# Kernel optimization log

Measured on AMD Instinct MI355X. Metric: run time of the kernel, lower is better.

Reference implementation:

```python
import jax, jax.numpy as jnp
import numpy as np

N = 32768      # points (multiple of block_size)
D = 32         # h_dim (dim_per_head, also token feature dim)
H = 8          # num_heads
C = 3          # n_hashes
BS = 128       # block_size
R = 3          # coords_dim
K = 8          # num_w_per_dist
NB = N // BS   # buckets
EPS_LN = 1e-5


def _ln(x, w, b):
    mu = x.mean(-1, keepdims=True)
    var = ((x - mu) ** 2).mean(-1, keepdims=True)
    return (x - mu) * jax.lax.rsqrt(var + EPS_LN) * w + b


def setup_inputs() -> dict:
    key = jax.random.key(0)
    ks = jax.random.split(key, 16)
    s = 0.05
    return {
        "x": jax.random.normal(ks[0], (N, D), jnp.float32),
        "coords": jax.random.uniform(ks[1], (N, R), jnp.float32),
        "combined_shifts": jax.random.randint(ks[2], (C, H, N), 0, 2048),
        "norm1_w": jnp.ones((D,), jnp.float32),
        "norm1_b": jnp.zeros((D,), jnp.float32),
        "wq": s * jax.random.normal(ks[3], (D, H * D), jnp.float32),
        "wk": s * jax.random.normal(ks[4], (D, H * D), jnp.float32),
        "wv": s * jax.random.normal(ks[5], (D, H * D), jnp.float32),
        "w_rpe_w": s * jax.random.normal(ks[6], (H * D, R * K), jnp.float32),
        "alpha": jax.random.normal(ks[7], (H, D + R, C), jnp.float32),  # E2LSH (frozen)
        "out_w": s * jax.random.normal(ks[8], (H * D, D), jnp.float32),
        "out_b": jnp.zeros((D,), jnp.float32),
        "norm2_w": jnp.ones((D,), jnp.float32),
        "norm2_b": jnp.zeros((D,), jnp.float32),
        "ff1_w": s * jax.random.normal(ks[9], (D, D), jnp.float32),
        "ff1_b": jnp.zeros((D,), jnp.float32),
        "ff2_w": s * jax.random.normal(ks[10], (D, D), jnp.float32),
        "ff2_b": jnp.zeros((D,), jnp.float32),
    }


def _to_buckets(v, perm):
    # v: [H, N, d], perm: [C, H, N] -> [C, H, NB, BS, d]
    g = jnp.take_along_axis(v[None], perm[..., None], axis=2)
    return g.reshape(C, H, NB, BS, v.shape[-1])


def _from_buckets(s, inv):
    # s: [C, H, NB, BS, d], inv: [C, H, N] -> [C, H, N, d]
    f = s.reshape(C, H, N, s.shape[-1])
    return jnp.take_along_axis(f, inv[..., None], axis=2)


def _hept_forward(x, coords, combined_shifts, norm1_w, norm1_b, wq, wk, wv,
                  w_rpe_w, alpha, out_w, out_b, norm2_w, norm2_b,
                  ff1_w, ff1_b, ff2_w, ff2_b):
    xn = _ln(x, norm1_w, norm1_b)
    q = (xn @ wq).reshape(N, H, D)
    k = (xn @ wk).reshape(N, H, D)
    v = (xn @ wv).reshape(N, H, D)

    # prep_qk: RPE-derived kernel coordinates
    w = w_rpe_w.reshape(H, D, R, K)                       # (h d) (r k) -> h d r k
    qw = jnp.exp(jnp.minimum(w.sum(axis=1), 50.0)).sum(-1)  # [H, R]
    sqrt_w_r = jnp.sqrt(2.0 * qw)[None] * coords[:, None]    # [N, H, R]
    q_hat = jnp.concatenate([q, sqrt_w_r], axis=-1)          # [N, H, D+R]
    k_hat = jnp.concatenate([k, sqrt_w_r], axis=-1)

    q_hat = jnp.transpose(q_hat, (1, 0, 2))  # [H, N, D+R]
    k_hat = jnp.transpose(k_hat, (1, 0, 2))
    val = jnp.transpose(v, (1, 0, 2))        # [H, N, D]

    # LSH hashing (no-grad in original; outputs only feed integer argsort)
    qh = jax.lax.stop_gradient(jnp.einsum('hnd,hdc->chn', q_hat, alpha))
    kh = jax.lax.stop_gradient(jnp.einsum('hnd,hdc->chn', k_hat, alpha))
    hi = jnp.maximum(qh.max(-1, keepdims=True), kh.max(-1, keepdims=True))
    lo = jnp.minimum(qh.min(-1, keepdims=True), kh.min(-1, keepdims=True))
    hash_shift = hi - lo                                    # [C, H, 1]
    shift = combined_shifts.astype(qh.dtype) * hash_shift
    q_pos = jnp.argsort(qh + shift, axis=-1)                # [C, H, N]
    k_pos = jnp.argsort(kh + shift, axis=-1)

    s_query = _to_buckets(q_hat, q_pos)
    s_key = _to_buckets(k_hat, k_pos)
    s_value = _to_buckets(val, k_pos)

    # kernelized exponential attention within buckets
    q_sq = -0.5 * (s_query ** 2).sum(-1, keepdims=True)
    k_sq = -0.5 * (s_key ** 2).sum(-1, keepdims=True)
    dists = jnp.einsum('chbid,chbjd->chbij', s_query, s_key)
    qk = jnp.exp(jnp.minimum(dists + q_sq + jnp.swapaxes(k_sq, -1, -2), 0.0))
    denom = qk.sum(-1, keepdims=True) + 1e-20
    so = jnp.einsum('chbij,chbjd->chbid', qk, s_value)

    q_rev = jnp.argsort(q_pos, axis=-1)  # inverse permutation
    o = _from_buckets(so, q_rev).sum(0)        # [H, N, D]
    logits = _from_buckets(denom, q_rev).sum(0)  # [H, N, 1]
    out = o / logits

    out = jnp.transpose(out, (1, 0, 2)).reshape(N, H * D) @ out_w + out_b
    x = x + out  # dropout is identity in eval
    xn2 = _ln(x, norm2_w, norm2_b)
    ff = jax.nn.silu(xn2 @ ff1_w + ff1_b) @ ff2_w + ff2_b
    return x + ff


def reference(x, coords, combined_shifts, norm1_w, norm1_b, wq, wk, wv,
              w_rpe_w, alpha, out_w, out_b, norm2_w, norm2_b,
              ff1_w, ff1_b, ff2_w, ff2_b):
    return _hept_forward(x, coords, combined_shifts, norm1_w, norm1_b, wq, wk, wv,
                         w_rpe_w, alpha, out_w, out_b, norm2_w, norm2_b,
                         ff1_w, ff1_b, ff2_w, ff2_b)
```

## Files before the change

### kernel.cpp

```cpp
#include <hip/hip_runtime.h>

#define NPTS 32768
#define DIM 32
#define NH 8
#define NC 3
#define BSZ 128
#define NB 256
#define DH 35
#define DP 36
#define NSEG 24

typedef unsigned long long ull;
typedef __attribute__((ext_vector_type(8))) short bf16x8;
typedef __attribute__((ext_vector_type(4))) float f32x4;

__device__ __forceinline__ unsigned fmap(float f){
  unsigned b = __float_as_uint(f);
  return (b & 0x80000000u) ? ~b : (b | 0x80000000u);
}
__device__ __forceinline__ float funmap(unsigned u){
  unsigned b = (u & 0x80000000u) ? (u & 0x7fffffffu) : ~u;
  return __uint_as_float(b);
}
__device__ __forceinline__ unsigned short f2bf(float f){
  unsigned u = __float_as_uint(f);
  u += 0x7fffu + ((u >> 16) & 1u);
  return (unsigned short)(u >> 16);
}
__device__ __forceinline__ float bf2f(unsigned short h){
  return __uint_as_float(((unsigned)h) << 16);
}
__device__ __forceinline__ unsigned cvtpk_bf16(float a, float b){
  unsigned r;
  asm("v_cvt_pk_bf16_f32 %0, %1, %2" : "=v"(r) : "v"(a), "v"(b));
  return r;
}

__device__ __forceinline__ void cswap(ull& a, ull& b, bool up){
  if ((a > b) == up){ ull t = a; a = b; b = t; }
}
__device__ __forceinline__ void bitonic8_initial(ull r[8], unsigned gbase){
  #pragma unroll
  for (int p = 0; p < 4; ++p){
    bool up = (((gbase + 2*p) & 2) == 0);
    cswap(r[2*p], r[2*p+1], up);
  }
  #pragma unroll
  for (int b = 0; b < 2; ++b){
    bool up = (((gbase + 4*b) & 4) == 0);
    cswap(r[4*b+0], r[4*b+2], up);
    cswap(r[4*b+1], r[4*b+3], up);
    cswap(r[4*b+0], r[4*b+1], up);
    cswap(r[4*b+2], r[4*b+3], up);
  }
  bool up = ((gbase & 8) == 0);
  #pragma unroll
  for (int i = 0; i < 4; ++i) cswap(r[i], r[i+4], up);
  #pragma unroll
  for (int b = 0; b < 2; ++b){
    cswap(r[4*b+0], r[4*b+2], up);
    cswap(r[4*b+1], r[4*b+3], up);
  }
  #pragma unroll
  for (int p = 0; p < 4; ++p) cswap(r[2*p], r[2*p+1], up);
}
__device__ __forceinline__ void bitonic8_finish(ull r[8], bool up){
  #pragma unroll
  for (int i = 0; i < 4; ++i) cswap(r[i], r[i+4], up);
  #pragma unroll
  for (int b = 0; b < 2; ++b){
    cswap(r[4*b+0], r[4*b+2], up);
    cswap(r[4*b+1], r[4*b+3], up);
  }
  #pragma unroll
  for (int p = 0; p < 4; ++p) cswap(r[2*p], r[2*p+1], up);
}

__global__ __launch_bounds__(256) void k_prep(const float* __restrict__ w_rpe,
        float* __restrict__ qw_sqrt, unsigned* __restrict__ slots_hi,
        unsigned* __restrict__ slots_lo){
  int tid = threadIdx.x;
  if (tid < NSEG){ slots_hi[tid] = 0u; slots_lo[tid] = 0xFFFFFFFFu; }
  __shared__ float S[24][8];
  if (tid < 192){
    int hr = tid >> 3, kk = tid & 7;
    int h = hr / 3, r = hr % 3;
    float s = 0.f;
    #pragma unroll
    for (int d = 0; d < DIM; ++d) s += w_rpe[(h*DIM + d)*24 + (r*8 + kk)];
    S[hr][kk] = expf(fminf(s, 50.f));
  }
  __syncthreads();
  if (tid < 24){
    float q = 0.f;
    #pragma unroll
    for (int kk = 0; kk < 8; ++kk) q += S[tid][kk];
    qw_sqrt[tid] = sqrtf(2.f * q);
  }
}

__global__ __launch_bounds__(256, 2) void k_qkv(const float* __restrict__ x,
        const float* __restrict__ n1w, const float* __restrict__ n1b,
        const float* __restrict__ coords, const float* __restrict__ wq,
        const float* __restrict__ wk, const float* __restrict__ wv,
        const float* __restrict__ qw_sqrt, const float* __restrict__ alpha,
        short* __restrict__ qpk, short* __restrict__ kpk, short* __restrict__ vbf,
        float* __restrict__ qh_buf, float* __restrict__ kh_buf,
        unsigned* __restrict__ slots_hi, unsigned* __restrict__ slots_lo){
  __shared__ float W[3][DIM][DIM];
  __shared__ float AL[DH][NC];
  __shared__ float LNW[DIM], LNB[DIM];
  __shared__ uint4 STG[3328];
  int h = blockIdx.y;
  int tid = threadIdx.x;
  for (int idx = tid; idx < 3*DIM*DIM; idx += 256){
    int which = idx >> 10, rem = idx & 1023;
    const float* src = which==0 ? wq : (which==1 ? wk : wv);
    W[which][rem>>5][rem&31] = src[(size_t)(rem>>5)*(NH*DIM) + h*DIM + (rem&31)];
  }
  for (int idx = tid; idx < DH*NC; idx += 256) ((float*)AL)[idx] = alpha[h*DH*NC + idx];
  if (tid < DIM) LNW[tid] = n1w[tid];
  else if (tid < 2*DIM) LNB[tid-DIM] = n1b[tid-DIM];
  __syncthreads();

  int base = blockIdx.x * 256;
  int n = base + tid;

  float xa[32];
  {
    const float4* p = (const float4*)(x + (size_t)n*DIM);
    float4 v[8]; float s = 0.f;
    #pragma unroll
    for (int u = 0; u < 8; ++u){ v[u]=p[u]; s += v[u].x+v[u].y+v[u].z+v[u].w; }
    float mu = s*(1.f/32.f), var = 0.f;
    #pragma unroll
    for (int u = 0; u < 8; ++u){
      float a0=v[u].x-mu,a1=v[u].y-mu,a2=v[u].z-mu,a3=v[u].w-mu;
      var += a0*a0+a1*a1+a2*a2+a3*a3;
    }
    var *= (1.f/32.f);
    float rs = rsqrtf(var + 1e-5f);
    #pragma unroll
    for (int u = 0; u < 8; ++u){
      xa[u*4+0]=(v[u].x-mu)*rs*LNW[u*4+0]+LNB[u*4+0];
      xa[u*4+1]=(v[u].y-mu)*rs*LNW[u*4+1]+LNB[u*4+1];
      xa[u*4+2]=(v[u].z-mu)*rs*LNW[u*4+2]+LNB[u*4+2];
      xa[u*4+3]=(v[u].w-mu)*rs*LNW[u*4+3]+LNB[u*4+3];
    }
  }

  float c0 = qw_sqrt[h*3+0]*coords[(size_t)n*3+0];
  float c1 = qw_sqrt[h*3+1]*coords[(size_t)n*3+1];
  float c2 = qw_sqrt[h*3+2]*coords[(size_t)n*3+2];
  float csq = c0*c0 + c1*c1 + c2*c2;

  uint2* rowp = (uint2*)&STG[tid*13];

  auto do_proj = [&](int which, float (&hp)[3], float& sq, bool dohash){
    #pragma unroll
    for (int j0 = 0; j0 < 32; j0 += 4){
      float4 a = {0,0,0,0};
      #pragma unroll
      for (int d = 0; d < 32; ++d){
        float4 w4 = *(const float4*)&W[which][d][j0];
        a.x += xa[d]*w4.x; a.y += xa[d]*w4.y; a.z += xa[d]*w4.z; a.w += xa[d]*w4.w;
      }
      if (dohash){
        sq += a.x*a.x; sq += a.y*a.y; sq += a.z*a.z; sq += a.w*a.w;
        #pragma unroll
        for (int c = 0; c < 3; ++c){
          float t = hp[c];
          t += a.x*AL[j0][c];   t += a.y*AL[j0+1][c];
          t += a.z*AL[j0+2][c]; t += a.w*AL[j0+3][c];
          hp[c] = t;
        }
      }
      unsigned short hx=f2bf(a.x),hy=f2bf(a.y),hz=f2bf(a.z),hw=f2bf(a.w);
      uint2 hv, lv;
      hv.x = (unsigned)hx | ((unsigned)hy<<16);
      hv.y = (unsigned)hz | ((unsigned)hw<<16);
      lv.x = (unsigned)f2bf(a.x-bf2f(hx)) | ((unsigned)f2bf(a.y-bf2f(hy))<<16);
      lv.y = (unsigned)f2bf(a.z-bf2f(hz)) | ((unsigned)f2bf(a.w-bf2f(hw))<<16);
      rowp[j0/4] = hv;
      rowp[12 + j0/4] = lv;
    }
  };
  auto stage_tail = [&](float x5, float x6){
    unsigned short h0=f2bf(c0),h1=f2bf(c1),h2=f2bf(c2),h5=f2bf(x5),h6=f2bf(x6);
    uint2 z2; z2.x=0; z2.y=0;
    uint2 hv0, hv1, lv0, lv1;
    hv0.x = (unsigned)h0 | ((unsigned)h1<<16);
    hv0.y = (unsigned)h2 | ((unsigned)h5<<16);
    hv1.x = (unsigned)h6; hv1.y = 0;
    lv0.x = (unsigned)f2bf(c0-bf2f(h0)) | ((unsigned)f2bf(c1-bf2f(h1))<<16);
    lv0.y = (unsigned)f2bf(c2-bf2f(h2)) | ((unsigned)f2bf(x5-bf2f(h5))<<16);
    lv1.x = (unsigned)f2bf(x6-bf2f(h6)); lv1.y = 0;
    rowp[8] = hv0; rowp[9] = hv1; rowp[10] = z2; rowp[11] = z2;
    rowp[20] = lv0; rowp[21] = lv1; rowp[22] = z2; rowp[23] = z2;
  };
  auto copy_qk = [&](short* gdst){
    uint4* du = (uint4*)gdst;
    #pragma unroll
    for (int it = 0; it < 12; ++it){
      unsigned g = (unsigned)it*256u + (unsigned)tid;
      unsigned row = g / 12u, k = g % 12u;
      du[g] = STG[row*13u + k];
    }
  };

  float qh[3]={0,0,0}, kh[3]={0,0,0};
  float sq = 0.f, dum = 0.f;

  do_proj(0, qh, sq, true);
  float qsq = -0.5f*(sq + csq);
  stage_tail(1.0f, qsq);
  __syncthreads();
  copy_qk(qpk + ((size_t)h*NPTS + base)*96);
  __syncthreads();

  sq = 0.f;
  do_proj(1, kh, sq, true);
  float ksq = -0.5f*(sq + csq);
  stage_tail(ksq, 1.0f);
  __syncthreads();
  copy_qk(kpk + ((size_t)h*NPTS + base)*96);
  __syncthreads();

  {
    float dh[3];
    uint2* rv = (uint2*)&STG[tid*5];
    #pragma unroll
    for (int j0 = 0; j0 < 32; j0 += 4){
      float4 a = {0,0,0,0};
      #pragma unroll
      for (int d = 0; d < 32; ++d){
        float4 w4 = *(const float4*)&W[2][d][j0];
        a.x += xa[d]*w4.x; a.y += xa[d]*w4.y; a.z += xa[d]*w4.z; a.w += xa[d]*w4.w;
      }
      uint2 hv;
      hv.x = (unsigned)f2bf(a.x) | ((unsigned)f2bf(a.y)<<16);
      hv.y = (unsigned)f2bf(a.z) | ((unsigned)f2bf(a.w)<<16);
      rv[j0/4] = hv;
    }
    (void)dh;
  }
  __syncthreads();
  {
    uint4* dv = (uint4*)(vbf + ((size_t)h*NPTS + base)*32);
    #pragma unroll
    for (int it = 0; it < 4; ++it){
      unsigned g = (unsigned)it*256u + (unsigned)tid;
      unsigned row = g >> 2, k = g & 3u;
      dv[g] = STG[row*5u + k];
    }
  }

  float mx[3], mn[3];
  #pragma unroll
  for (int c = 0; c < 3; ++c){
    float qa_ = qh[c];
    qa_ += c0*AL[32][c]; qa_ += c1*AL[33][c]; qa_ += c2*AL[34][c];
    float ka_ = kh[c];
    ka_ += c0*AL[32][c]; ka_ += c1*AL[33][c]; ka_ += c2*AL[34][c];
    qh_buf[(size_t)(c*NH + h)*NPTS + n] = qa_;
    kh_buf[(size_t)(c*NH + h)*NPTS + n] = ka_;
    mx[c] = fmaxf(qa_, ka_);
    mn[c] = fminf(qa_, ka_);
  }
  #pragma unroll
  for (int c = 0; c < 3; ++c){
    float mx_ = mx[c], mn_ = mn[c];
    #pragma unroll
    for (int off = 1; off <= 32; off <<= 1){
      mx_ = fmaxf(mx_, __shfl_xor(mx_, off));
      mn_ = fminf(mn_, __shfl_xor(mn_, off));
    }
    if ((tid & 63) == 0){
      atomicMax(&slots_hi[c*NH + h], fmap(mx_));
      atomicMin(&slots_lo[c*NH + h], fmap(mn_));
    }
  }
  (void)dum;
}

__global__ __launch_bounds__(1024) void k_sort_pack_local(
        const float* __restrict__ qh_buf, const float* __restrict__ kh_buf,
        const int* __restrict__ shifts,
        const unsigned* __restrict__ slots_hi, const unsigned* __restrict__ slots_lo,
        ull* __restrict__ packed){
  __shared__ ull ld[9216];
  int chunk = blockIdx.x;
  int lst = chunk >> 2;
  int seg = lst < NSEG ? lst : lst - NSEG;
  const float* buf = lst < NSEG ? qh_buf : kh_buf;
  unsigned coff = (unsigned)(chunk & 3) * 8192u;
  float hs = funmap(slots_hi[seg]) - funmap(slots_lo[seg]);
  unsigned tid = threadIdx.x;

  {
    ull r[8];
    unsigned gb = coff + 8u*tid;
    #pragma unroll
    for (int e = 0; e < 8; ++e){
      unsigned n = gb + e;
      size_t gi = (size_t)seg*NPTS + n;
      float key = buf[gi] + (float)shifts[gi] * hs;
      r[e] = ((ull)fmap(key) << 32) | n;
    }
    bitonic8_initial(r, gb);
    #pragma unroll
    for (int e = 0; e < 8; ++e) ld[9u*tid + e] = r[e];
  }
  __syncthreads();

  for (unsigned k = 16; k <= 8192u; k <<= 1){
    for (unsigned j = k >> 1; j >= 8; j >>= 1){
      #pragma unroll
      for (int it = 0; it < 4; ++it){
        unsigned p = tid + 1024u*it;
        unsigned i  = ((p & ~(j-1)) << 1) | (p & (j-1));
        unsigned x2 = i | j;
        bool up = (((coff + i) & k) == 0);
        unsigned pi = i + (i>>3), px = x2 + (x2>>3);
        ull a = ld[pi], b2 = ld[px];
        if ((a > b2) == up){ ld[pi] = b2; ld[px] = a; }
      }
      __syncthreads();
    }
    {
      ull r[8];
      #pragma unroll
      for (int e = 0; e < 8; ++e) r[e] = ld[9u*tid + e];
      bool up = (((coff + 8u*tid) & k) == 0);
      bitonic8_finish(r, up);
      #pragma unroll
      for (int e = 0; e < 8; ++e) ld[9u*tid + e] = r[e];
    }
    __syncthreads();
  }
  size_t base = (size_t)lst*NPTS + coff;
  for (unsigned idx = tid; idx < 8192; idx += 1024)
    packed[base + idx] = ld[idx + (idx>>3)];
}

__global__ __launch_bounds__(1024) void k_sort_local(ull* __restrict__ data,
        unsigned k_lo, unsigned k_hi){
  __shared__ ull ld[9216];
  int chunk = blockIdx.x;
  size_t base = (size_t)chunk * 8192;
  unsigned coff = (unsigned)(chunk & 3) * 8192u;
  unsigned tid = threadIdx.x;
  for (unsigned idx = tid; idx < 8192; idx += 1024)
    ld[idx + (idx>>3)] = data[base + idx];
  __syncthreads();
  for (unsigned k = k_lo; k <= k_hi; k <<= 1){
    unsigned j0 = (k >> 1) < 4096u ? (k >> 1) : 4096u;
    for (unsigned j = j0; j >= 8; j >>= 1){
      #pragma unroll
      for (int it = 0; it < 4; ++it){
        unsigned p = tid + 1024u*it;
        unsigned i  = ((p & ~(j-1)) << 1) | (p & (j-1));
        unsigned x2 = i | j;
        bool up = (((coff + i) & k) == 0);
        unsigned pi = i + (i>>3), px = x2 + (x2>>3);
        ull a = ld[pi], b2 = ld[px];
        if ((a > b2) == up){ ld[pi] = b2; ld[px] = a; }
      }
      __syncthreads();
    }
    {
      ull r[8];
      #pragma unroll
      for (int e = 0; e < 8; ++e) r[e] = ld[9u*tid + e];
      bool up = (((coff + 8u*tid) & k) == 0);
      bitonic8_finish(r, up);
      #pragma unroll
      for (int e = 0; e < 8; ++e) ld[9u*tid + e] = r[e];
    }
    __syncthreads();
  }
  for (unsigned idx = tid; idx < 8192; idx += 1024)
    data[base + idx] = ld[idx + (idx>>3)];
}

__global__ __launch_bounds__(256) void k_sort_global(ull* __restrict__ data,
        unsigned k, unsigned j){
  unsigned t = blockIdx.x*256 + threadIdx.x;
  unsigned seg = t >> 14;
  unsigned p = t & 16383u;
  unsigned i  = ((p & ~(j-1)) << 1) | (p & (j-1));
  unsigned x2 = i | j;
  size_t base = (size_t)seg << 15;
  bool up = ((i & k) == 0);
  ull a = data[base + i], b = data[base + x2];
  if ((a > b) == up){ data[base + i] = b; data[base + x2] = a; }
}

__global__ __launch_bounds__(256) void k_sort_global2(ull* __restrict__ data){
  unsigned t = blockIdx.x*256 + threadIdx.x;
  unsigned seg = t >> 13;
  unsigned i = t & 8191u;
  size_t base = ((size_t)seg << 15) + i;
  ull e0 = data[base], e1 = data[base + 8192], e2 = data[base + 16384], e3 = data[base + 24576];
  cswap(e0, e2, true); cswap(e1, e3, true);
  cswap(e0, e1, true); cswap(e2, e3, true);
  data[base] = e0; data[base + 8192] = e1;
  data[base + 16384] = e2; data[base + 24576] = e3;
}

__global__ __launch_bounds__(512, 8) void k_attn(const short* __restrict__ qpk,
        const short* __restrict__ kpk, const short* __restrict__ vbf,
        const ull* __restrict__ packed, float* __restrict__ o_acc,
        float* __restrict__ logit_acc){
  __shared__ short KP[16384];
  __shared__ short Vt[4096];

  int t = threadIdx.x;
  int blk = blockIdx.x;
  int seg = blk >> 8;
  int b = blk & 255;
  int h = seg & 7;
  const ull* pq = packed + ((size_t)seg << 15) + (size_t)b*BSZ;
  const ull* pk = packed + ((size_t)(NSEG + seg) << 15) + (size_t)b*BSZ;

  int lane = t & 63;
  int w = t >> 6;
  int l15 = lane & 15, g = lane >> 4;
  int qrow = 16*w + l15;

  unsigned iqr = (unsigned)(pq[qrow] & 0xffffffffull);
  const short* qrp = qpk + ((size_t)h*NPTS + iqr)*96;
  bf16x8 qh0 = *(const bf16x8*)&qrp[8*g];
  bf16x8 ql0 = *(const bf16x8*)&qrp[48 + 8*g];
  bf16x8 qh1 = (bf16x8){0,0,0,0,0,0,0,0};
  bf16x8 ql1 = (bf16x8){0,0,0,0,0,0,0,0};
  if (g < 2){
    qh1 = *(const bf16x8*)&qrp[32 + 8*g];
    ql1 = *(const bf16x8*)&qrp[80 + 8*g];
  }

  {
    int r = t >> 2;
    int qd = t & 3;
    unsigned ik = (unsigned)(pk[r] & 0xffffffffull);
    int rowbase = r*64;
    int sw = (r & 7) << 3;
    const short* krp = kpk + ((size_t)h*NPTS + ik)*96;
    if (qd < 3){
      bf16x8 h0 = *(const bf16x8*)&krp[16*qd];
      bf16x8 h1 = *(const bf16x8*)&krp[16*qd + 8];
      bf16x8 l0 = *(const bf16x8*)&krp[48 + 16*qd];
      bf16x8 l1 = *(const bf16x8*)&krp[56 + 16*qd];
      *(bf16x8*)&KP[rowbase + ((16*qd) ^ sw)] = h0;
      *(bf16x8*)&KP[rowbase + ((16*qd + 8) ^ sw)] = h1;
      *(bf16x8*)&KP[8192 + rowbase + ((16*qd) ^ sw)] = l0;
      *(bf16x8*)&KP[8192 + rowbase + ((16*qd + 8) ^ sw)] = l1;
    } else {
      bf16x8 z = (bf16x8){0,0,0,0,0,0,0,0};
      *(bf16x8*)&KP[rowbase + (48 ^ sw)] = z;
      *(bf16x8*)&KP[rowbase + (56 ^ sw)] = z;
      *(bf16x8*)&KP[8192 + rowbase + (48 ^ sw)] = z;
      *(bf16x8*)&KP[8192 + rowbase + (56 ^ sw)] = z;
    }
    const short* vrp = vbf + ((size_t)h*NPTS + ik)*32 + 8*qd;
    bf16x8 vv = *(const bf16x8*)vrp;
    #pragma unroll
    for (int d2 = 0; d2 < 8; ++d2){
      int vd = 8*qd + d2;
      Vt[vd*128 + (r ^ ((vd & 7) << 3))] = vv[d2];
    }
  }
  __syncthreads();

  f32x4 acc[8];
  #pragma unroll
  for (int kt = 0; kt < 8; ++kt) acc[kt] = (f32x4){0.f,0.f,0.f,0.f};
  #pragma unroll
  for (int kt = 0; kt < 8; ++kt){
    int krow = 16*kt + l15;
    int base = krow*64;
    int sw = (krow & 7) << 3;
    bf16x8 ah0 = *(const bf16x8*)&KP[base + ((8*g) ^ sw)];
    bf16x8 ah1 = *(const bf16x8*)&KP[base + ((32 + 8*g) ^ sw)];
    bf16x8 al0 = *(const bf16x8*)&KP[8192 + base + ((8*g) ^ sw)];
    bf16x8 al1 = *(const bf16x8*)&KP[8192 + base + ((32 + 8*g) ^ sw)];
    f32x4 c = acc[kt];
    c = __builtin_amdgcn_mfma_f32_16x16x32_bf16(ah0, qh0, c, 0, 0, 0);
    c = __builtin_amdgcn_mfma_f32_16x16x32_bf16(ah1, qh1, c, 0, 0, 0);
    c = __builtin_amdgcn_mfma_f32_16x16x32_bf16(al0, qh0, c, 0, 0, 0);
    c = __builtin_amdgcn_mfma_f32_16x16x32_bf16(al1, qh1, c, 0, 0, 0);
    c = __builtin_amdgcn_mfma_f32_16x16x32_bf16(ah0, ql0, c, 0, 0, 0);
    c = __builtin_amdgcn_mfma_f32_16x16x32_bf16(ah1, ql1, c, 0, 0, 0);
    acc[kt] = c;
  }

  __syncthreads();

  int qsw = (qrow & 7) << 3;
  float dena = 0.f;
  #pragma unroll
  for (int kt = 0; kt < 8; ++kt){
    f32x4 c = acc[kt];
    float p0 = __expf(fminf(c[0], 0.f));
    float p1 = __expf(fminf(c[1], 0.f));
    float p2 = __expf(fminf(c[2], 0.f));
    float p3 = __expf(fminf(c[3], 0.f));
    dena += p0 + p1 + p2 + p3;
    int key = 16*kt + 4*g;
    uint2 pv;
    pv.x = cvtpk_bf16(p0, p1);
    pv.y = cvtpk_bf16(p2, p3);
    *(uint2*)&KP[qrow*128 + (key ^ qsw)] = pv;
  }

  f32x4 oacc[2];
  oacc[0] = (f32x4){0.f,0.f,0.f,0.f};
  oacc[1] = (f32x4){0.f,0.f,0.f,0.f};
  #pragma unroll
  for (int ks = 0; ks < 4; ++ks){
    bf16x8 pA = *(const bf16x8*)&KP[qrow*128 + ((32*ks + 8*g) ^ qsw)];
    #pragma unroll
    for (int nt = 0; nt < 2; ++nt){
      int vd = 16*nt + l15;
      bf16x8 vB = *(const bf16x8*)&Vt[vd*128 + ((32*ks + 8*g) ^ ((vd&7)<<3))];
      oacc[nt] = __builtin_amdgcn_mfma_f32_16x16x32_bf16(pA, vB, oacc[nt], 0, 0, 0);
    }
  }

  {
    float d = dena;
    d += __shfl_xor(d, 16);
    d += __shfl_xor(d, 32);
    if (lane < 16) atomicAdd(&logit_acc[(size_t)h*NPTS + iqr], d + 1e-20f);
  }
  #pragma unroll
  for (int nt = 0; nt < 2; ++nt){
    f32x4 c = oacc[nt];
    #pragma unroll
    for (int r = 0; r < 4; ++r){
      unsigned iq = (unsigned)__shfl((int)iqr, 4*g + r);
      atomicAdd(&o_acc[((size_t)h*NPTS + iq)*DIM + 16*nt + l15], c[r]);
    }
  }
}

__global__ __launch_bounds__(256) void k_final(const float* __restrict__ x,
        const float* __restrict__ o_acc, const float* __restrict__ logit_acc,
        const float* __restrict__ out_w, const float* __restrict__ out_b,
        const float* __restrict__ n2w, const float* __restrict__ n2b,
        const float* __restrict__ f1w, const float* __restrict__ f1b,
        const float* __restrict__ f2w, const float* __restrict__ f2b,
        float* __restrict__ out){
  __shared__ float OW[256][32];
  __shared__ float F1[32][32];
  __shared__ float F2[32][32];
  int tid = threadIdx.x;
  for (int idx = tid; idx < 256*32; idx += 256) OW[idx/32][idx%32] = out_w[idx];
  for (int idx = tid; idx < 1024; idx += 256){
    F1[idx/32][idx%32] = f1w[idx];
    F2[idx/32][idx%32] = f2w[idx];
  }
  __syncthreads();
  int n = blockIdx.x*256 + tid;
  float attn[32];
  #pragma unroll
  for (int j = 0; j < 32; ++j) attn[j] = out_b[j];
  for (int h = 0; h < 8; ++h){
    float inv = 1.f / logit_acc[(size_t)h*NPTS + n];
    const float4* orow = (const float4*)(o_acc + ((size_t)h*NPTS + n)*DIM);
    #pragma unroll
    for (int u = 0; u < 8; ++u){
      float4 ov = orow[u];
      float vals[4] = {ov.x*inv, ov.y*inv, ov.z*inv, ov.w*inv};
      #pragma unroll
      for (int s = 0; s < 4; ++s){
        const float* wrow = &OW[h*32 + u*4 + s][0];
        #pragma unroll
        for (int j = 0; j < 32; ++j) attn[j] += vals[s] * wrow[j];
      }
    }
  }
  const float* xp = x + (size_t)n*DIM;
  float xr[32]; float s = 0.f;
  #pragma unroll
  for (int d = 0; d < 32; ++d){ xr[d] = xp[d] + attn[d]; s += xr[d]; }
  float mu = s * (1.f/32.f);
  float var = 0.f;
  #pragma unroll
  for (int d = 0; d < 32; ++d){ float dx = xr[d]-mu; var += dx*dx; }
  var *= (1.f/32.f);
  float rs = rsqrtf(var + 1e-5f);
  float xn2[32];
  #pragma unroll
  for (int d = 0; d < 32; ++d) xn2[d] = (xr[d]-mu)*rs*n2w[d] + n2b[d];
  float z[32];
  #pragma unroll
  for (int j = 0; j < 32; ++j) z[j] = f1b[j];
  #pragma unroll
  for (int d = 0; d < 32; ++d){
    float xd = xn2[d];
    const float* wrow = &F1[d][0];
    #pragma unroll
    for (int j = 0; j < 32; ++j) z[j] += xd * wrow[j];
  }
  #pragma unroll
  for (int j = 0; j < 32; ++j) z[j] = z[j] / (1.f + __expf(-z[j]));
  float y[32];
  #pragma unroll
  for (int d = 0; d < 32; ++d) y[d] = f2b[d];
  #pragma unroll
  for (int j = 0; j < 32; ++j){
    float zj = z[j];
    const float* wrow = &F2[j][0];
    #pragma unroll
    for (int d = 0; d < 32; ++d) y[d] += zj * wrow[d];
  }
  float* op = out + (size_t)n*DIM;
  #pragma unroll
  for (int d = 0; d < 32; ++d) op[d] = xr[d] + y[d];
}

extern "C" void kernel_launch(void* const* d_in, const int* in_sizes, int n_in,
                              void* d_out, int out_size, void* d_ws, size_t ws_size,
                              hipStream_t stream){
  const float* x      = (const float*)d_in[0];
  const float* coords = (const float*)d_in[1];
  const int*   shifts = (const int*)d_in[2];
  const float* n1w    = (const float*)d_in[3];
  const float* n1b    = (const float*)d_in[4];
  const float* wq     = (const float*)d_in[5];
  const float* wk     = (const float*)d_in[6];
  const float* wv     = (const float*)d_in[7];
  const float* w_rpe  = (const float*)d_in[8];
  const float* alpha  = (const float*)d_in[9];
  const float* out_w  = (const float*)d_in[10];
  const float* out_b  = (const float*)d_in[11];
  const float* n2w    = (const float*)d_in[12];
  const float* n2b    = (const float*)d_in[13];
  const float* f1w    = (const float*)d_in[14];
  const float* f1b    = (const float*)d_in[15];
  const float* f2w    = (const float*)d_in[16];
  const float* f2b    = (const float*)d_in[17];
  float* out = (float*)d_out;

  char* ws = (char*)d_ws;
  size_t off = 0;
  auto alloc = [&](size_t bytes){ size_t o = off; off += (bytes + 255) & ~(size_t)255; return o; };
  float*    qw_sqrt   = (float*)   (ws + alloc(24*4));
  unsigned* slots_hi  = (unsigned*)(ws + alloc(24*4));
  unsigned* slots_lo  = (unsigned*)(ws + alloc(24*4));
  short*    qpk       = (short*)   (ws + alloc((size_t)NH*NPTS*96*2));
  short*    kpk       = (short*)   (ws + alloc((size_t)NH*NPTS*96*2));
  short*    vbf       = (short*)   (ws + alloc((size_t)NH*NPTS*32*2));
  float*    qh_buf    = (float*)   (ws + alloc((size_t)NSEG*NPTS*4));
  float*    kh_buf    = (float*)   (ws + alloc((size_t)NSEG*NPTS*4));
  ull*      packed    = (ull*)     (ws + alloc((size_t)2*NSEG*NPTS*8));
  float*    o_acc     = (float*)   (ws + alloc((size_t)NH*NPTS*DIM*4));
  float*    logit_acc = (float*)   (ws + alloc((size_t)NH*NPTS*4));
  if (off > ws_size) return;

  hipMemsetAsync(o_acc, 0, (size_t)NH*NPTS*DIM*4, stream);
  hipMemsetAsync(logit_acc, 0, (size_t)NH*NPTS*4, stream);

  k_prep<<<1, 256, 0, stream>>>(w_rpe, qw_sqrt, slots_hi, slots_lo);
  k_qkv<<<dim3(NPTS/256, NH), 256, 0, stream>>>(x, n1w, n1b, coords, wq, wk, wv,
                                                qw_sqrt, alpha, qpk, kpk, vbf,
                                                qh_buf, kh_buf, slots_hi, slots_lo);
  k_sort_pack_local<<<2*NSEG*4, 1024, 0, stream>>>(qh_buf, kh_buf, shifts,
                                                   slots_hi, slots_lo, packed);
  k_sort_global<<<(2*NSEG*16384)/256, 256, 0, stream>>>(packed, 16384u, 8192u);
  k_sort_local<<<2*NSEG*4, 1024, 0, stream>>>(packed, 16384u, 16384u);
  k_sort_global2<<<(2*NSEG*8192)/256, 256, 0, stream>>>(packed);
  k_sort_local<<<2*NSEG*4, 1024, 0, stream>>>(packed, 32768u, 32768u);

  k_attn<<<NSEG*NB, 512, 0, stream>>>(qpk, kpk, vbf, packed, o_acc, logit_acc);
  k_final<<<NPTS/256, 256, 0, stream>>>(x, o_acc, logit_acc, out_w, out_b,
                                        n2w, n2b, f1w, f1b, f2w, f2b, out);
}
```

Baseline: 442.7 us.

## Replace atomic scatter of attention outputs with sorted-order stores and gather

The attention kernel now writes per-bucket outputs and denominators in sorted order (outputs in bf16) instead of atomically adding into per-point accumulators. A new kernel builds the inverse permutation, and the final kernel gathers the three hash contributions per head via that index. This removes the memsets and the float atomics, at the cost of an extra gather pass and bf16 rounding of the partial outputs. Separately, the QKV kernel splits each point across two threads (half the output columns each), using less shared memory and a higher occupancy hint.

```diff
diff --git a/kernel.cpp b/kernel.cpp
--- a/kernel.cpp
+++ b/kernel.cpp
@@ -99,7 +99,7 @@
   }
 }
 
-__global__ __launch_bounds__(256, 2) void k_qkv(const float* __restrict__ x,
+__global__ __launch_bounds__(256, 4) void k_qkv(const float* __restrict__ x,
         const float* __restrict__ n1w, const float* __restrict__ n1b,
         const float* __restrict__ coords, const float* __restrict__ wq,
         const float* __restrict__ wk, const float* __restrict__ wv,
@@ -110,7 +110,7 @@
   __shared__ float W[3][DIM][DIM];
   __shared__ float AL[DH][NC];
   __shared__ float LNW[DIM], LNB[DIM];
-  __shared__ uint4 STG[3328];
+  __shared__ uint4 STG[1664];
   int h = blockIdx.y;
   int tid = threadIdx.x;
   for (int idx = tid; idx < 3*DIM*DIM; idx += 256){
@@ -123,15 +123,17 @@
   else if (tid < 2*DIM) LNB[tid-DIM] = n1b[tid-DIM];
   __syncthreads();
 
-  int base = blockIdx.x * 256;
-  int n = base + tid;
+  int base = blockIdx.x * 128;
+  int tl = tid >> 1;
+  int p  = tid & 1;
+  int n  = base + tl;
 
   float xa[32];
   {
-    const float4* p = (const float4*)(x + (size_t)n*DIM);
+    const float4* pp = (const float4*)(x + (size_t)n*DIM);
     float4 v[8]; float s = 0.f;
     #pragma unroll
-    for (int u = 0; u < 8; ++u){ v[u]=p[u]; s += v[u].x+v[u].y+v[u].z+v[u].w; }
+    for (int u = 0; u < 8; ++u){ v[u]=pp[u]; s += v[u].x+v[u].y+v[u].z+v[u].w; }
     float mu = s*(1.f/32.f), var = 0.f;
     #pragma unroll
     for (int u = 0; u < 8; ++u){
@@ -154,11 +156,12 @@
   float c2 = qw_sqrt[h*3+2]*coords[(size_t)n*3+2];
   float csq = c0*c0 + c1*c1 + c2*c2;
 
-  uint2* rowp = (uint2*)&STG[tid*13];
+  uint2* rowp = (uint2*)&STG[tl*13];
 
   auto do_proj = [&](int which, float (&hp)[3], float& sq, bool dohash){
     #pragma unroll
-    for (int j0 = 0; j0 < 32; j0 += 4){
+    for (int j0l = 0; j0l < 16; j0l += 4){
+      int j0 = p*16 + j0l;
       float4 a = {0,0,0,0};
       #pragma unroll
       for (int d = 0; d < 32; ++d){
@@ -181,8 +184,8 @@
       hv.y = (unsigned)hz | ((unsigned)hw<<16);
       lv.x = (unsigned)f2bf(a.x-bf2f(hx)) | ((unsigned)f2bf(a.y-bf2f(hy))<<16);
       lv.y = (unsigned)f2bf(a.z-bf2f(hz)) | ((unsigned)f2bf(a.w-bf2f(hw))<<16);
-      rowp[j0/4] = hv;
-      rowp[12 + j0/4] = lv;
+      rowp[j0>>2] = hv;
+      rowp[12 + (j0>>2)] = lv;
     }
   };
   auto stage_tail = [&](float x5, float x6){
@@ -201,7 +204,7 @@
   auto copy_qk = [&](short* gdst){
     uint4* du = (uint4*)gdst;
     #pragma unroll
-    for (int it = 0; it < 12; ++it){
+    for (int it = 0; it < 6; ++it){
       unsigned g = (unsigned)it*256u + (unsigned)tid;
       unsigned row = g / 12u, k = g % 12u;
       du[g] = STG[row*13u + k];
@@ -209,28 +212,34 @@
   };
 
   float qh[3]={0,0,0}, kh[3]={0,0,0};
-  float sq = 0.f, dum = 0.f;
+  float sq = 0.f;
 
   do_proj(0, qh, sq, true);
-  float qsq = -0.5f*(sq + csq);
-  stage_tail(1.0f, qsq);
+  {
+    float sqt = sq + __shfl_xor(sq, 1);
+    float qsq = -0.5f*(sqt + csq);
+    if (p == 0) stage_tail(1.0f, qsq);
+  }
   __syncthreads();
   copy_qk(qpk + ((size_t)h*NPTS + base)*96);
   __syncthreads();
 
   sq = 0.f;
   do_proj(1, kh, sq, true);
-  float ksq = -0.5f*(sq + csq);
-  stage_tail(ksq, 1.0f);
+  {
+    float sqt = sq + __shfl_xor(sq, 1);
+    float ksq = -0.5f*(sqt + csq);
+    if (p == 0) stage_tail(ksq, 1.0f);
+  }
   __syncthreads();
   copy_qk(kpk + ((size_t)h*NPTS + base)*96);
   __syncthreads();
 
   {
-    float dh[3];
-    uint2* rv = (uint2*)&STG[tid*5];
-    #pragma unroll
-    for (int j0 = 0; j0 < 32; j0 += 4){
+    uint2* rv = (uint2*)&STG[tl*5];
+    #pragma unroll
+    for (int j0l = 0; j0l < 16; j0l += 4){
+      int j0 = p*16 + j0l;
       float4 a = {0,0,0,0};
       #pragma unroll
       for (int d = 0; d < 32; ++d){
@@ -240,15 +249,14 @@
       uint2 hv;
       hv.x = (unsigned)f2bf(a.x) | ((unsigned)f2bf(a.y)<<16);
       hv.y = (unsigned)f2bf(a.z) | ((unsigned)f2bf(a.w)<<16);
-      rv[j0/4] = hv;
-    }
-    (void)dh;
+      rv[j0>>2] = hv;
+    }
   }
   __syncthreads();
   {
     uint4* dv = (uint4*)(vbf + ((size_t)h*NPTS + base)*32);
     #pragma unroll
-    for (int it = 0; it < 4; ++it){
+    for (int it = 0; it < 2; ++it){
       unsigned g = (unsigned)it*256u + (unsigned)tid;
       unsigned row = g >> 2, k = g & 3u;
       dv[g] = STG[row*5u + k];
@@ -258,14 +266,16 @@
   float mx[3], mn[3];
   #pragma unroll
   for (int c = 0; c < 3; ++c){
-    float qa_ = qh[c];
-    qa_ += c0*AL[32][c]; qa_ += c1*AL[33][c]; qa_ += c2*AL[34][c];
-    float ka_ = kh[c];
-    ka_ += c0*AL[32][c]; ka_ += c1*AL[33][c]; ka_ += c2*AL[34][c];
-    qh_buf[(size_t)(c*NH + h)*NPTS + n] = qa_;
-    kh_buf[(size_t)(c*NH + h)*NPTS + n] = ka_;
-    mx[c] = fmaxf(qa_, ka_);
-    mn[c] = fminf(qa_, ka_);
+    float qt = qh[c] + __shfl_xor(qh[c], 1);
+    qt += c0*AL[32][c]; qt += c1*AL[33][c]; qt += c2*AL[34][c];
+    float kt = kh[c] + __shfl_xor(kh[c], 1);
+    kt += c0*AL[32][c]; kt += c1*AL[33][c]; kt += c2*AL[34][c];
+    if (p == 0){
+      qh_buf[(size_t)(c*NH + h)*NPTS + n] = qt;
+      kh_buf[(size_t)(c*NH + h)*NPTS + n] = kt;
+    }
+    mx[c] = fmaxf(qt, kt);
+    mn[c] = fminf(qt, kt);
   }
   #pragma unroll
   for (int c = 0; c < 3; ++c){
@@ -280,7 +290,6 @@
       atomicMin(&slots_lo[c*NH + h], fmap(mn_));
     }
   }
-  (void)dum;
 }
 
 __global__ __launch_bounds__(1024) void k_sort_pack_local(
@@ -408,10 +417,19 @@
   data[base + 16384] = e2; data[base + 24576] = e3;
 }
 
+__global__ __launch_bounds__(256) void k_qrev(const ull* __restrict__ packed,
+        unsigned* __restrict__ qrev){
+  unsigned t = blockIdx.x*256 + threadIdx.x;
+  unsigned seg = t >> 15;
+  unsigned pos = t & 32767u;
+  unsigned idx = (unsigned)(packed[(size_t)seg*NPTS + pos] & 0xffffffffull);
+  qrev[(size_t)seg*NPTS + idx] = pos;
+}
+
 __global__ __launch_bounds__(512, 8) void k_attn(const short* __restrict__ qpk,
         const short* __restrict__ kpk, const short* __restrict__ vbf,
-        const ull* __restrict__ packed, float* __restrict__ o_acc,
-        float* __restrict__ logit_acc){
+        const ull* __restrict__ packed, unsigned short* __restrict__ o_sorted,
+        float* __restrict__ den_sorted){
   __shared__ short KP[16384];
   __shared__ short Vt[4096];
 
@@ -531,21 +549,23 @@
     float d = dena;
     d += __shfl_xor(d, 16);
     d += __shfl_xor(d, 32);
-    if (lane < 16) atomicAdd(&logit_acc[(size_t)h*NPTS + iqr], d + 1e-20f);
-  }
+    if (lane < 16) den_sorted[(size_t)seg*NPTS + (size_t)b*BSZ + 16*w + l15] = d;
+  }
+  size_t obase = ((size_t)seg*NPTS + (size_t)b*BSZ)*32;
   #pragma unroll
   for (int nt = 0; nt < 2; ++nt){
     f32x4 c = oacc[nt];
     #pragma unroll
     for (int r = 0; r < 4; ++r){
-      unsigned iq = (unsigned)__shfl((int)iqr, 4*g + r);
-      atomicAdd(&o_acc[((size_t)h*NPTS + iq)*DIM + 16*nt + l15], c[r]);
+      int row = 16*w + 4*g + r;
+      o_sorted[obase + (size_t)row*32 + 16*nt + l15] = f2bf(c[r]);
     }
   }
 }
 
 __global__ __launch_bounds__(256) void k_final(const float* __restrict__ x,
-        const float* __restrict__ o_acc, const float* __restrict__ logit_acc,
+        const unsigned short* __restrict__ o_sorted, const float* __restrict__ den_sorted,
+        const unsigned* __restrict__ qrev,
         const float* __restrict__ out_w, const float* __restrict__ out_b,
         const float* __restrict__ n2w, const float* __restrict__ n2b,
         const float* __restrict__ f1w, const float* __restrict__ f1b,
@@ -566,18 +586,36 @@
   #pragma unroll
   for (int j = 0; j < 32; ++j) attn[j] = out_b[j];
   for (int h = 0; h < 8; ++h){
-    float inv = 1.f / logit_acc[(size_t)h*NPTS + n];
-    const float4* orow = (const float4*)(o_acc + ((size_t)h*NPTS + n)*DIM);
-    #pragma unroll
-    for (int u = 0; u < 8; ++u){
-      float4 ov = orow[u];
-      float vals[4] = {ov.x*inv, ov.y*inv, ov.z*inv, ov.w*inv};
-      #pragma unroll
-      for (int s = 0; s < 4; ++s){
-        const float* wrow = &OW[h*32 + u*4 + s][0];
-        #pragma unroll
-        for (int j = 0; j < 32; ++j) attn[j] += vals[s] * wrow[j];
+    float osum[32];
+    #pragma unroll
+    for (int d = 0; d < 32; ++d) osum[d] = 0.f;
+    float den = 3e-20f;
+    #pragma unroll
+    for (int c = 0; c < 3; ++c){
+      size_t sbase = (size_t)(c*NH + h)*NPTS;
+      unsigned pp = qrev[sbase + n];
+      den += den_sorted[sbase + pp];
+      const unsigned short* orow = o_sorted + (sbase + pp)*32;
+      #pragma unroll
+      for (int u = 0; u < 4; ++u){
+        uint4 v = *(const uint4*)&orow[u*8];
+        osum[u*8+0] += bf2f((unsigned short)(v.x & 0xffffu));
+        osum[u*8+1] += bf2f((unsigned short)(v.x >> 16));
+        osum[u*8+2] += bf2f((unsigned short)(v.y & 0xffffu));
+        osum[u*8+3] += bf2f((unsigned short)(v.y >> 16));
+        osum[u*8+4] += bf2f((unsigned short)(v.z & 0xffffu));
+        osum[u*8+5] += bf2f((unsigned short)(v.z >> 16));
+        osum[u*8+6] += bf2f((unsigned short)(v.w & 0xffffu));
+        osum[u*8+7] += bf2f((unsigned short)(v.w >> 16));
       }
+    }
+    float inv = 1.f / den;
+    #pragma unroll
+    for (int d = 0; d < 32; ++d){
+      float val = osum[d]*inv;
+      const float* wrow = &OW[h*32 + d][0];
+      #pragma unroll
+      for (int j = 0; j < 32; ++j) attn[j] += val * wrow[j];
     }
   }
   const float* xp = x + (size_t)n*DIM;
@@ -652,18 +690,16 @@
   short*    qpk       = (short*)   (ws + alloc((size_t)NH*NPTS*96*2));
   short*    kpk       = (short*)   (ws + alloc((size_t)NH*NPTS*96*2));
   short*    vbf       = (short*)   (ws + alloc((size_t)NH*NPTS*32*2));
+  ull*      packed    = (ull*)     (ws + alloc((size_t)2*NSEG*NPTS*8));
+  unsigned short* o_sorted = (unsigned short*)(ws + alloc((size_t)NSEG*NPTS*32*2));
   float*    qh_buf    = (float*)   (ws + alloc((size_t)NSEG*NPTS*4));
   float*    kh_buf    = (float*)   (ws + alloc((size_t)NSEG*NPTS*4));
-  ull*      packed    = (ull*)     (ws + alloc((size_t)2*NSEG*NPTS*8));
-  float*    o_acc     = (float*)   (ws + alloc((size_t)NH*NPTS*DIM*4));
-  float*    logit_acc = (float*)   (ws + alloc((size_t)NH*NPTS*4));
   if (off > ws_size) return;
-
-  hipMemsetAsync(o_acc, 0, (size_t)NH*NPTS*DIM*4, stream);
-  hipMemsetAsync(logit_acc, 0, (size_t)NH*NPTS*4, stream);
+  float*    den_sorted = qh_buf;
+  unsigned* qrev       = (unsigned*)kh_buf;
 
   k_prep<<<1, 256, 0, stream>>>(w_rpe, qw_sqrt, slots_hi, slots_lo);
-  k_qkv<<<dim3(NPTS/256, NH), 256, 0, stream>>>(x, n1w, n1b, coords, wq, wk, wv,
+  k_qkv<<<dim3(NPTS/128, NH), 256, 0, stream>>>(x, n1w, n1b, coords, wq, wk, wv,
                                                 qw_sqrt, alpha, qpk, kpk, vbf,
                                                 qh_buf, kh_buf, slots_hi, slots_lo);
   k_sort_pack_local<<<2*NSEG*4, 1024, 0, stream>>>(qh_buf, kh_buf, shifts,
@@ -673,7 +709,8 @@
   k_sort_global2<<<(2*NSEG*8192)/256, 256, 0, stream>>>(packed);
   k_sort_local<<<2*NSEG*4, 1024, 0, stream>>>(packed, 32768u, 32768u);
 
-  k_attn<<<NSEG*NB, 512, 0, stream>>>(qpk, kpk, vbf, packed, o_acc, logit_acc);
-  k_final<<<NPTS/256, 256, 0, stream>>>(x, o_acc, logit_acc, out_w, out_b,
+  k_qrev<<<(NSEG*NPTS)/256, 256, 0, stream>>>(packed, qrev);
+  k_attn<<<NSEG*NB, 512, 0, stream>>>(qpk, kpk, vbf, packed, o_sorted, den_sorted);
+  k_final<<<NPTS/256, 256, 0, stream>>>(x, o_sorted, den_sorted, qrev, out_w, out_b,
                                         n2w, n2b, f1w, f1b, f2w, f2b, out);
 }
```

New measurement: 860.2 us. 1.94x slower.

## Replace scattered atomic accumulation with sorted bf16 outputs and inverse-permutation gather

Applied to the files above, without the earlier changes.

The attention kernel no longer scatters fp32 atomicAdds into per-point accumulators. It writes its outputs in bucket-sorted order as bf16, with the denominators stored as plain floats. A new kernel builds the inverse permutation, and the final kernel gathers and sums the three hash rounds per head before the output projection. This removes the two memsets and the atomic traffic, but adds a gather pass and rounds the attention output to bf16 before normalization.

```diff
diff --git a/kernel.cpp b/kernel.cpp
--- a/kernel.cpp
+++ b/kernel.cpp
@@ -227,7 +227,6 @@
   __syncthreads();
 
   {
-    float dh[3];
     uint2* rv = (uint2*)&STG[tid*5];
     #pragma unroll
     for (int j0 = 0; j0 < 32; j0 += 4){
@@ -242,7 +241,6 @@
       hv.y = (unsigned)f2bf(a.z) | ((unsigned)f2bf(a.w)<<16);
       rv[j0/4] = hv;
     }
-    (void)dh;
   }
   __syncthreads();
   {
@@ -408,10 +406,19 @@
   data[base + 16384] = e2; data[base + 24576] = e3;
 }
 
+__global__ __launch_bounds__(256) void k_qrev(const ull* __restrict__ packed,
+        unsigned* __restrict__ qrev){
+  unsigned t = blockIdx.x*256 + threadIdx.x;
+  unsigned seg = t >> 15;
+  unsigned pos = t & 32767u;
+  unsigned idx = (unsigned)(packed[(size_t)seg*NPTS + pos] & 0xffffffffull);
+  qrev[(size_t)seg*NPTS + idx] = pos;
+}
+
 __global__ __launch_bounds__(512, 8) void k_attn(const short* __restrict__ qpk,
         const short* __restrict__ kpk, const short* __restrict__ vbf,
-        const ull* __restrict__ packed, float* __restrict__ o_acc,
-        float* __restrict__ logit_acc){
+        const ull* __restrict__ packed, unsigned short* __restrict__ o_sorted,
+        float* __restrict__ den_sorted){
   __shared__ short KP[16384];
   __shared__ short Vt[4096];
 
@@ -531,21 +538,23 @@
     float d = dena;
     d += __shfl_xor(d, 16);
     d += __shfl_xor(d, 32);
-    if (lane < 16) atomicAdd(&logit_acc[(size_t)h*NPTS + iqr], d + 1e-20f);
-  }
+    if (lane < 16) den_sorted[(size_t)seg*NPTS + (size_t)b*BSZ + 16*w + l15] = d;
+  }
+  size_t obase = ((size_t)seg*NPTS + (size_t)b*BSZ)*32;
   #pragma unroll
   for (int nt = 0; nt < 2; ++nt){
     f32x4 c = oacc[nt];
     #pragma unroll
     for (int r = 0; r < 4; ++r){
-      unsigned iq = (unsigned)__shfl((int)iqr, 4*g + r);
-      atomicAdd(&o_acc[((size_t)h*NPTS + iq)*DIM + 16*nt + l15], c[r]);
+      int row = 16*w + 4*g + r;
+      o_sorted[obase + (size_t)row*32 + 16*nt + l15] = f2bf(c[r]);
     }
   }
 }
 
 __global__ __launch_bounds__(256) void k_final(const float* __restrict__ x,
-        const float* __restrict__ o_acc, const float* __restrict__ logit_acc,
+        const unsigned short* __restrict__ o_sorted, const float* __restrict__ den_sorted,
+        const unsigned* __restrict__ qrev,
         const float* __restrict__ out_w, const float* __restrict__ out_b,
         const float* __restrict__ n2w, const float* __restrict__ n2b,
         const float* __restrict__ f1w, const float* __restrict__ f1b,
@@ -566,18 +575,36 @@
   #pragma unroll
   for (int j = 0; j < 32; ++j) attn[j] = out_b[j];
   for (int h = 0; h < 8; ++h){
-    float inv = 1.f / logit_acc[(size_t)h*NPTS + n];
-    const float4* orow = (const float4*)(o_acc + ((size_t)h*NPTS + n)*DIM);
-    #pragma unroll
-    for (int u = 0; u < 8; ++u){
-      float4 ov = orow[u];
-      float vals[4] = {ov.x*inv, ov.y*inv, ov.z*inv, ov.w*inv};
-      #pragma unroll
-      for (int s = 0; s < 4; ++s){
-        const float* wrow = &OW[h*32 + u*4 + s][0];
-        #pragma unroll
-        for (int j = 0; j < 32; ++j) attn[j] += vals[s] * wrow[j];
+    float osum[32];
+    #pragma unroll
+    for (int d = 0; d < 32; ++d) osum[d] = 0.f;
+    float den = 3e-20f;
+    #pragma unroll
+    for (int c = 0; c < 3; ++c){
+      size_t sbase = (size_t)(c*NH + h)*NPTS;
+      unsigned pp = qrev[sbase + n];
+      den += den_sorted[sbase + pp];
+      const unsigned short* orow = o_sorted + (sbase + pp)*32;
+      #pragma unroll
+      for (int u = 0; u < 4; ++u){
+        uint4 v = *(const uint4*)&orow[u*8];
+        osum[u*8+0] += bf2f((unsigned short)(v.x & 0xffffu));
+        osum[u*8+1] += bf2f((unsigned short)(v.x >> 16));
+        osum[u*8+2] += bf2f((unsigned short)(v.y & 0xffffu));
+        osum[u*8+3] += bf2f((unsigned short)(v.y >> 16));
+        osum[u*8+4] += bf2f((unsigned short)(v.z & 0xffffu));
+        osum[u*8+5] += bf2f((unsigned short)(v.z >> 16));
+        osum[u*8+6] += bf2f((unsigned short)(v.w & 0xffffu));
+        osum[u*8+7] += bf2f((unsigned short)(v.w >> 16));
       }
+    }
+    float inv = 1.f / den;
+    #pragma unroll
+    for (int d = 0; d < 32; ++d){
+      float val = osum[d]*inv;
+      const float* wrow = &OW[h*32 + d][0];
+      #pragma unroll
+      for (int j = 0; j < 32; ++j) attn[j] += val * wrow[j];
     }
   }
   const float* xp = x + (size_t)n*DIM;
@@ -652,15 +679,13 @@
   short*    qpk       = (short*)   (ws + alloc((size_t)NH*NPTS*96*2));
   short*    kpk       = (short*)   (ws + alloc((size_t)NH*NPTS*96*2));
   short*    vbf       = (short*)   (ws + alloc((size_t)NH*NPTS*32*2));
+  ull*      packed    = (ull*)     (ws + alloc((size_t)2*NSEG*NPTS*8));
+  unsigned short* o_sorted = (unsigned short*)(ws + alloc((size_t)NSEG*NPTS*32*2));
   float*    qh_buf    = (float*)   (ws + alloc((size_t)NSEG*NPTS*4));
   float*    kh_buf    = (float*)   (ws + alloc((size_t)NSEG*NPTS*4));
-  ull*      packed    = (ull*)     (ws + alloc((size_t)2*NSEG*NPTS*8));
-  float*    o_acc     = (float*)   (ws + alloc((size_t)NH*NPTS*DIM*4));
-  float*    logit_acc = (float*)   (ws + alloc((size_t)NH*NPTS*4));
   if (off > ws_size) return;
-
-  hipMemsetAsync(o_acc, 0, (size_t)NH*NPTS*DIM*4, stream);
-  hipMemsetAsync(logit_acc, 0, (size_t)NH*NPTS*4, stream);
+  float*    den_sorted = qh_buf;
+  unsigned* qrev       = (unsigned*)kh_buf;
 
   k_prep<<<1, 256, 0, stream>>>(w_rpe, qw_sqrt, slots_hi, slots_lo);
   k_qkv<<<dim3(NPTS/256, NH), 256, 0, stream>>>(x, n1w, n1b, coords, wq, wk, wv,
@@ -673,7 +698,8 @@
   k_sort_global2<<<(2*NSEG*8192)/256, 256, 0, stream>>>(packed);
   k_sort_local<<<2*NSEG*4, 1024, 0, stream>>>(packed, 32768u, 32768u);
 
-  k_attn<<<NSEG*NB, 512, 0, stream>>>(qpk, kpk, vbf, packed, o_acc, logit_acc);
-  k_final<<<NPTS/256, 256, 0, stream>>>(x, o_acc, logit_acc, out_w, out_b,
+  k_qrev<<<(NSEG*NPTS)/256, 256, 0, stream>>>(packed, qrev);
+  k_attn<<<NSEG*NB, 512, 0, stream>>>(qpk, kpk, vbf, packed, o_sorted, den_sorted);
+  k_final<<<NPTS/256, 256, 0, stream>>>(x, o_sorted, den_sorted, qrev, out_w, out_b,
                                         n2w, n2b, f1w, f1b, f2w, f2b, out);
 }
```

Measured after the change: 423.7 us. -4.3%, faster.
